# Kernel tuning notes

Hardware: AMD Instinct MI355X
Metric: run time of the kernel (lower is better)

The kernel has to match this reference:

```python
import jax, jax.numpy as jnp
import numpy as np

B, S, D = 2, 2048, 1024
H = 16
DH = D // H


def setup_inputs() -> dict:
    key = jax.random.key(0)
    ks = jax.random.split(key, 6)
    scale = 0.02
    X = jax.random.normal(ks[0], (B, S, D), dtype=jnp.float32)
    W_q = jax.random.normal(ks[1], (D, D), dtype=jnp.float32) * scale
    W_k = jax.random.normal(ks[2], (D, D), dtype=jnp.float32) * scale
    W_v = jax.random.normal(ks[3], (D, D), dtype=jnp.float32) * scale
    W_o = jax.random.normal(ks[4], (D, D), dtype=jnp.float32) * scale
    b_o = jax.random.normal(ks[5], (D,), dtype=jnp.float32) * scale
    return {"X": X, "W_q": W_q, "W_k": W_k, "W_v": W_v, "W_o": W_o, "b_o": b_o}


def reference(X, W_q, W_k, W_v, W_o, b_o):
    batch, seq, _ = X.shape
    # project and split heads -> [B, H, S, DH]
    Q = (X @ W_q).reshape(batch, seq, H, DH).transpose(0, 2, 1, 3)
    K = (X @ W_k).reshape(batch, seq, H, DH).transpose(0, 2, 1, 3)
    V = (X @ W_v).reshape(batch, seq, H, DH).transpose(0, 2, 1, 3)
    # scores [B, H, S, S]
    scores = jnp.einsum("bhqd,bhkd->bhqk", Q, K)
    causal = jnp.tril(jnp.ones((seq, seq), dtype=bool))  # True = keep
    scores = jnp.where(causal, scores, -jnp.inf)
    scores = scores / jnp.sqrt(jnp.float32(DH))
    weights = jax.nn.softmax(scores, axis=-1)
    # dropout_p = 0.0 -> identity
    ctx = jnp.einsum("bhqk,bhkd->bhqd", weights, V)
    ctx = ctx.transpose(0, 2, 1, 3).reshape(batch, seq, D)
    return ctx @ W_o + b_o
```

## Files before the change

### kernel.cpp

```cpp
#include <hip/hip_runtime.h>
#include <hip/hip_bf16.h>

#define S 2048
#define D 1024
#define NH 16
#define DH 64
#define M_TOT 4096

typedef float f32x4 __attribute__((ext_vector_type(4)));
typedef float f32x16 __attribute__((ext_vector_type(16)));
typedef __bf16 bf16x8 __attribute__((ext_vector_type(8)));

static __device__ __forceinline__ ushort f2bf(float f) {
    unsigned u = __float_as_uint(f);
    u += 0x7fffu + ((u >> 16) & 1u);
    return (ushort)(u >> 16);
}

static __device__ __forceinline__ int cvtpk_bf16(float lo, float hi) {
    int r;
    asm("v_cvt_pk_bf16_f32 %0, %1, %2" : "=v"(r) : "v"(lo), "v"(hi));
    return r;
}

static __device__ __forceinline__ void plswap(int& a, int& b) {
    asm("v_permlane32_swap_b32 %0, %1" : "+v"(a), "+v"(b));
}

static __device__ __forceinline__ float xhalf_add(float x) {
    return x + __shfl_xor(x, 32);
}

static __device__ __forceinline__ void gload16(const ushort* g, ushort* l) {
    __builtin_amdgcn_global_load_lds(
        (const __attribute__((address_space(1))) void*)g,
        (__attribute__((address_space(3))) void*)l, 16, 0, 0);
}

template<int N> static __device__ __forceinline__ void waitvm() {
    if constexpr (N == 0) asm volatile("s_waitcnt vmcnt(0)" ::: "memory");
    else if constexpr (N == 3) asm volatile("s_waitcnt vmcnt(3)" ::: "memory");
    else if constexpr (N == 4) asm volatile("s_waitcnt vmcnt(4)" ::: "memory");
}
static __device__ __forceinline__ void waitlgkm0() {
    asm volatile("s_waitcnt lgkmcnt(0)" ::: "memory");
}
static __device__ __forceinline__ void rawbar() {
    __builtin_amdgcn_s_barrier();
    __builtin_amdgcn_sched_barrier(0);
}

__global__ void k_convert(const float* __restrict__ src, ushort* __restrict__ dst, int n4) {
    int i = blockIdx.x * blockDim.x + threadIdx.x;
    int stride = gridDim.x * blockDim.x;
    for (int idx = i; idx < n4; idx += stride) {
        float4 v = ((const float4*)src)[idx];
        ushort4 o;
        o.x = f2bf(v.x); o.y = f2bf(v.y); o.z = f2bf(v.z); o.w = f2bf(v.w);
        ((ushort4*)dst)[idx] = o;
    }
}

__global__ void k_transposeW(const float* __restrict__ w0, const float* __restrict__ w1,
                             const float* __restrict__ w2, ushort* __restrict__ dst,
                             float scale0) {
    __shared__ float tile[32][33];
    int z = blockIdx.z;
    const float* src = (z == 0) ? w0 : (z == 1) ? w1 : w2;
    float scl = (z == 0) ? scale0 : 1.0f;
    int zoff = z * 1024;
    int bn = blockIdx.x * 32;
    int bk = blockIdx.y * 32;
    int tx = threadIdx.x & 31, ty = threadIdx.x >> 5;
    #pragma unroll
    for (int i = 0; i < 32; i += 8)
        tile[ty + i][tx] = src[(size_t)(bk + ty + i) * D + bn + tx];
    __syncthreads();
    #pragma unroll
    for (int i = 0; i < 32; i += 8)
        dst[(size_t)(zoff + bn + ty + i) * D + bk + tx] = f2bf(tile[tx][ty + i] * scl);
}

template<int MF>
__global__ __launch_bounds__(256) void k_gemm(
    const ushort* __restrict__ A, const ushort* __restrict__ Bt,
    ushort* __restrict__ Qd, ushort* __restrict__ Kd, ushort* __restrict__ Vd,
    float* __restrict__ Od, const float* __restrict__ bias, int mode)
{
    constexpr int BM = MF * 32;
    constexpr int ASZ = BM * 32;
    constexpr int BSZ = 128 * 32;
    constexpr int NL = (MF == 4) ? 4 : 3;
    __shared__ ushort SH[2 * ASZ + 2 * BSZ];
    ushort* As = SH;
    ushort* Bs = SH + 2 * ASZ;

    int tid = threadIdx.x, wave = tid >> 6, lane = tid & 63;
    int wm = (wave >> 1) * (MF * 16), wn = (wave & 1) * 64;
    int bm = blockIdx.x * BM, bn0 = blockIdx.y * 128;
    int lr = lane & 15, lk = (lane >> 4) * 8;
    int rr = (lane >> 4) * 4;
    f32x4 acc[MF][4] = {};

    const ushort* Ap0 = A + (size_t)(bm + (tid >> 2)) * D + (tid & 3) * 8;
    const ushort* Ap1 = A + (size_t)(bm + ((tid + 256) >> 2)) * D + (tid & 3) * 8;
    const ushort* Bp0 = Bt + (size_t)(bn0 + (tid >> 2)) * D + (tid & 3) * 8;
    const ushort* Bp1 = Bt + (size_t)(bn0 + ((tid + 256) >> 2)) * D + (tid & 3) * 8;
    ushort* la0 = As + tid * 8;
    ushort* la1 = As + (tid + 256) * 8;
    ushort* lb0 = Bs + tid * 8;
    ushort* lb1 = Bs + (tid + 256) * 8;

    auto stage = [&](int k, int buf) {
        int go = k * 32;
        gload16(Ap0 + go, la0 + buf * ASZ);
        if constexpr (MF == 4) gload16(Ap1 + go, la1 + buf * ASZ);
        gload16(Bp0 + go, lb0 + buf * BSZ);
        gload16(Bp1 + go, lb1 + buf * BSZ);
    };

    constexpr int NK = D / 32;
    stage(0, 0);
    stage(1, 1);

    #pragma unroll 1
    for (int k0 = 0; k0 < NK; ++k0) {
        if (k0 + 1 < NK) waitvm<NL>(); else waitvm<0>();
        rawbar();
        const ushort* Ac = As + (k0 & 1) * ASZ;
        const ushort* Bc = Bs + (k0 & 1) * BSZ;
        bf16x8 af[MF], bfr[4];
        #pragma unroll
        for (int m = 0; m < MF; ++m) af[m] = *(const bf16x8*)&Ac[(wm + m * 16 + lr) * 32 + lk];
        #pragma unroll
        for (int n = 0; n < 4; ++n) bfr[n] = *(const bf16x8*)&Bc[(wn + n * 16 + lr) * 32 + lk];
        waitlgkm0();
        rawbar();
        if (k0 + 2 < NK) stage(k0 + 2, k0 & 1);
        __builtin_amdgcn_s_setprio(1);
        #pragma unroll
        for (int m = 0; m < MF; ++m)
            #pragma unroll
            for (int n = 0; n < 4; ++n)
                acc[m][n] = __builtin_amdgcn_mfma_f32_16x16x32_bf16(af[m], bfr[n], acc[m][n], 0, 0, 0);
        __builtin_amdgcn_s_setprio(0);
    }

    if (mode == 0) {
        ushort* E = SH;
        const bool isV = (blockIdx.y >= 16);
        ushort* DstQK = (blockIdx.y < 8) ? Qd : Kd;
        int bnc = (blockIdx.y & 7) * 128;
        int b = bm >> 11;
        #pragma unroll 1
        for (int hh2 = 0; hh2 < 2; ++hh2) {
            __syncthreads();
            if (wm == hh2 * 64) {
                if (!isV) {
                    #pragma unroll
                    for (int m = 0; m < MF; ++m)
                        #pragma unroll
                        for (int n = 0; n < 4; ++n)
                            #pragma unroll
                            for (int r = 0; r < 4; ++r)
                                E[(m * 16 + rr + r) * 136 + wn + n * 16 + lr] = f2bf(acc[m][n][r]);
                } else {
                    #pragma unroll
                    for (int m = 0; m < MF; ++m)
                        #pragma unroll
                        for (int n = 0; n < 4; ++n) {
                            ushort4 w;
                            w.x = f2bf(acc[m][n][0]); w.y = f2bf(acc[m][n][1]);
                            w.z = f2bf(acc[m][n][2]); w.w = f2bf(acc[m][n][3]);
                            *(ushort4*)&E[(wn + n * 16 + lr) * 72 + m * 16 + rr] = w;
                        }
                }
            }
            __syncthreads();
            if (!isV) {
                #pragma unroll
                for (int p = 0; p < 4; ++p) {
                    int rloc = (tid >> 4) + p * 16;
                    int c8 = (tid & 15) * 8;
                    int4 v = *(const int4*)&E[rloc * 136 + c8];
                    int gm = bm + hh2 * 64 + rloc;
                    int ss = gm & (S - 1);
                    int n = bnc + c8;
                    int hh = n >> 6, dd = n & 63;
                    *(int4*)&DstQK[((size_t)(b * NH + hh) * S + ss) * DH + dd] = v;
                }
            } else {
                #pragma unroll
                for (int p = 0; p < 4; ++p) {
                    int c = tid >> 1;
                    int chunk = 2 * p + (tid & 1);
                    int4 v = *(const int4*)&E[c * 72 + chunk * 8];
                    int n = bnc + c;
                    int hh = n >> 6, dd = n & 63;
                    int gm = bm + hh2 * 64 + chunk * 8;
                    int ss = gm & (S - 1);
                    *(int4*)&Vd[((size_t)(b * NH + hh) * DH + dd) * S + ss] = v;
                }
            }
        }
    } else {
        #pragma unroll
        for (int m = 0; m < MF; ++m) {
            #pragma unroll
            for (int n = 0; n < 4; ++n) {
                int gn = bn0 + wn + n * 16 + lr;
                float bv = bias[gn];
                #pragma unroll
                for (int r = 0; r < 4; ++r) {
                    int gm = bm + wm + m * 16 + rr + r;
                    Od[(size_t)gm * D + gn] = acc[m][n][r] + bv;
                }
            }
        }
    }
}

__global__ __launch_bounds__(256, 4) void k_attn(
    const ushort* __restrict__ Qh, const ushort* __restrict__ Kh,
    const ushort* __restrict__ Vt, ushort* __restrict__ ctx)
{
    __shared__ ushort Ks[2][4096];
    __shared__ ushort Vs[2][4096];

    int bid = blockIdx.x;
    int r_ = bid >> 8, c_ = bid & 255;
    int qt = (r_ & 1) ? (c_ >> 3) : 31 - (c_ >> 3);
    int bh = (c_ & 7) + 8 * r_;

    int tid = threadIdx.x;
    int wave = tid >> 6, lane = tid & 63;
    int lo5 = lane & 31, hi = lane >> 5;
    int qs = wave >> 1, kp = wave & 1;
    int rxl = lo5 & 7;
    int b = bh >> 4, h = bh & (NH - 1);

    const ushort* Qp = Qh + (size_t)bh * S * DH;
    const ushort* Kp = Kh + (size_t)bh * S * DH;
    const ushort* Vp = Vt + (size_t)bh * DH * S;

    int q0 = qt * 64, q0w = q0 + qs * 32, qg = q0w + lo5;
    int nt = qt + 1;

    bf16x8 qf[4];
    #pragma unroll
    for (int ks = 0; ks < 4; ++ks)
        qf[ks] = *(const bf16x8*)&Qp[(size_t)qg * DH + ks * 16 + hi * 8];

    int koff[4], vof[2];
    #pragma unroll
    for (int ks = 0; ks < 4; ++ks)
        koff[ks] = (kp * 32 + lo5) * 64 + (((2 * ks + hi) ^ rxl) << 3);
    #pragma unroll
    for (int kc = 0; kc < 2; ++kc)
        vof[kc] = lo5 * 64 + (((kp * 4 + 2 * kc + hi) ^ rxl) << 3);

    int p0 = tid, p1 = tid + 256;
    int kr0 = p0 >> 3, kc0 = ((p0 & 7) ^ (kr0 & 7)) << 3;
    int kr1 = p1 >> 3, kc1 = ((p1 & 7) ^ (kr1 & 7)) << 3;
    const ushort* gkA = Kp + (size_t)kr0 * DH + kc0;
    const ushort* gkB = Kp + (size_t)kr1 * DH + kc1;
    const ushort* gvA = Vp + (size_t)kr0 * S + kc0;
    const ushort* gvB = Vp + (size_t)kr1 * S + kc1;
    ushort* lk0 = &Ks[0][p0 * 8];
    ushort* lk1 = &Ks[0][p1 * 8];
    ushort* lv0 = &Vs[0][p0 * 8];
    ushort* lv1 = &Vs[0][p1 * 8];

    auto stage = [&](int t, int buf) {
        int ko = t * (64 * DH);
        int vo = t * 64;
        int lo = buf * 4096;
        gload16(gkA + ko, lk0 + lo);
        gload16(gkB + ko, lk1 + lo);
        gload16(gvA + vo, lv0 + lo);
        gload16(gvB + vo, lv1 + lo);
    };

    f32x16 oacc[2] = {};
    float l = 0.f;

    stage(0, 0);
    if (nt > 1) stage(1, 1);

    #pragma unroll 1
    for (int t = 0; t < nt; ++t) {
        if (t + 1 < nt) waitvm<4>(); else waitvm<0>();
        rawbar();
        bool fullmask = (t == qt) && (kp == 1) && (qs == 0);
        if (!fullmask) {
            const ushort* KsC = &Ks[t & 1][0];
            const ushort* VsC = &Vs[t & 1][0];
            f32x16 sc = (f32x16)(0.f);
            __builtin_amdgcn_s_setprio(1);
            #pragma unroll
            for (int ks = 0; ks < 4; ++ks) {
                bf16x8 kf = *(const bf16x8*)&KsC[koff[ks]];
                sc = __builtin_amdgcn_mfma_f32_32x32x16_bf16(kf, qf[ks], sc, 0, 0, 0);
            }
            __builtin_amdgcn_s_setprio(0);

            int kv0 = t * 64;
            if (t == qt && !(kp == 0 && qs == 1)) {
                #pragma unroll
                for (int r2 = 0; r2 < 16; ++r2) {
                    int kvg = kv0 + kp * 32 + ((r2 & 3) + 8 * (r2 >> 2) + 4 * hi);
                    sc[r2] = (kvg > qg) ? -1e30f : sc[r2];
                }
            }
            float sum = 0.f;
            #pragma unroll
            for (int r2 = 0; r2 < 16; ++r2) {
                float p = exp2f(sc[r2]);
                sc[r2] = p;
                sum += p;
            }
            l += sum;

            bf16x8 pb[2];
            {
                int a0 = cvtpk_bf16(sc[0], sc[1]);
                int b0 = cvtpk_bf16(sc[4], sc[5]);
                plswap(a0, b0);
                int a1 = cvtpk_bf16(sc[2], sc[3]);
                int b1 = cvtpk_bf16(sc[6], sc[7]);
                plswap(a1, b1);
                int4 w0; w0.x = a0; w0.y = a1; w0.z = b0; w0.w = b1;
                pb[0] = *(bf16x8*)&w0;
                int a2 = cvtpk_bf16(sc[8], sc[9]);
                int b2 = cvtpk_bf16(sc[12], sc[13]);
                plswap(a2, b2);
                int a3 = cvtpk_bf16(sc[10], sc[11]);
                int b3 = cvtpk_bf16(sc[14], sc[15]);
                plswap(a3, b3);
                int4 w1; w1.x = a2; w1.y = a3; w1.z = b2; w1.w = b3;
                pb[1] = *(bf16x8*)&w1;
            }

            __builtin_amdgcn_s_setprio(1);
            #pragma unroll
            for (int kc = 0; kc < 2; ++kc) {
                bf16x8 vf0 = *(const bf16x8*)&VsC[vof[kc]];
                oacc[0] = __builtin_amdgcn_mfma_f32_32x32x16_bf16(vf0, pb[kc], oacc[0], 0, 0, 0);
                bf16x8 vf1 = *(const bf16x8*)&VsC[vof[kc] + 32 * 64];
                oacc[1] = __builtin_amdgcn_mfma_f32_32x32x16_bf16(vf1, pb[kc], oacc[1], 0, 0, 0);
            }
            __builtin_amdgcn_s_setprio(0);
        }
        waitlgkm0();
        rawbar();
        if (t + 2 < nt) stage(t + 2, t & 1);
    }

    l = xhalf_add(l);

    float4* scr4 = (float4*)&Ks[0][0];
    float* ls = (float*)&Vs[0][0];
    int row = qs * 64 + lane;
    if (kp == 1) {
        #pragma unroll
        for (int sub = 0; sub < 2; ++sub)
            #pragma unroll
            for (int cc = 0; cc < 4; ++cc) {
                float4 v4;
                v4.x = oacc[sub][4 * cc + 0];
                v4.y = oacc[sub][4 * cc + 1];
                v4.z = oacc[sub][4 * cc + 2];
                v4.w = oacc[sub][4 * cc + 3];
                scr4[row * 8 + ((sub * 4 + cc) ^ (row & 7))] = v4;
            }
        ls[row] = l;
    }
    __syncthreads();
    if (kp == 0) {
        float inv = 1.0f / (l + ls[row]);
        ushort* cp = ctx + (size_t)(b * S + qg) * D + h * DH;
        #pragma unroll
        for (int sub = 0; sub < 2; ++sub) {
            #pragma unroll
            for (int cc = 0; cc < 4; ++cc) {
                float4 v4 = scr4[row * 8 + ((sub * 4 + cc) ^ (row & 7))];
                float o0 = (oacc[sub][4 * cc + 0] + v4.x) * inv;
                float o1 = (oacc[sub][4 * cc + 1] + v4.y) * inv;
                float o2 = (oacc[sub][4 * cc + 2] + v4.z) * inv;
                float o3 = (oacc[sub][4 * cc + 3] + v4.w) * inv;
                int dh = 8 * cc + 4 * hi + 32 * sub;
                int2 w2; w2.x = cvtpk_bf16(o0, o1); w2.y = cvtpk_bf16(o2, o3);
                *(int2*)&cp[dh] = w2;
            }
        }
    }
}

extern "C" void kernel_launch(void* const* d_in, const int* in_sizes, int n_in,
                              void* d_out, int out_size, void* d_ws, size_t ws_size,
                              hipStream_t stream) {
    const float* X   = (const float*)d_in[0];
    const float* W_q = (const float*)d_in[1];
    const float* W_k = (const float*)d_in[2];
    const float* W_v = (const float*)d_in[3];
    const float* W_o = (const float*)d_in[4];
    const float* b_o = (const float*)d_in[5];
    float* out = (float*)d_out;

    ushort* Xb    = (ushort*)d_ws;
    ushort* Wqkvt = Xb    + (size_t)M_TOT * D;
    ushort* Wot   = Wqkvt + (size_t)3 * D * D;
    ushort* Qh    = Wot   + (size_t)D * D;
    ushort* Kh    = Qh    + (size_t)M_TOT * D;
    ushort* Vtr   = Kh    + (size_t)M_TOT * D;
    ushort* Ctx   = Vtr   + (size_t)M_TOT * D;

    k_convert<<<dim3(2048), dim3(256), 0, stream>>>(X, Xb, M_TOT * D / 4);
    k_transposeW<<<dim3(32, 32, 3), dim3(256), 0, stream>>>(W_q, W_k, W_v, Wqkvt, 0.18033688011112042f);
    k_transposeW<<<dim3(32, 32, 1), dim3(256), 0, stream>>>(W_o, W_o, W_o, Wot, 1.0f);

    k_gemm<4><<<dim3(32, 24), dim3(256), 0, stream>>>(Xb, Wqkvt, Qh, Kh, Vtr, nullptr, nullptr, 0);

    k_attn<<<dim3(1024), dim3(256), 0, stream>>>(Qh, Kh, Vtr, Ctx);

    k_gemm<2><<<dim3(64, 8), dim3(256), 0, stream>>>(Ctx, Wot, nullptr, nullptr, nullptr, out, b_o, 1);
}
```

Measured before the change: 114.0 us.

## Load K and V fragments directly from global memory instead of LDS staging

The attention loop drops the double-buffered LDS staging of K and V tiles, and with it the per-iteration barriers. Each wave now reads its MFMA K and V fragments straight from global memory, relying on the cache for reuse across waves. The exp-sum reduction becomes a tree. This removes the barrier and LDS traffic but exposes global load latency every iteration with no prefetching, and duplicates K/V loads across waves.

```diff
diff --git a/kernel.cpp b/kernel.cpp
--- a/kernel.cpp
+++ b/kernel.cpp
@@ -224,8 +224,8 @@
     const ushort* __restrict__ Qh, const ushort* __restrict__ Kh,
     const ushort* __restrict__ Vt, ushort* __restrict__ ctx)
 {
-    __shared__ ushort Ks[2][4096];
-    __shared__ ushort Vs[2][4096];
+    __shared__ float4 scr4[128 * 8];
+    __shared__ float ls[128];
 
     int bid = blockIdx.x;
     int r_ = bid >> 8, c_ = bid & 255;
@@ -236,7 +236,6 @@
     int wave = tid >> 6, lane = tid & 63;
     int lo5 = lane & 31, hi = lane >> 5;
     int qs = wave >> 1, kp = wave & 1;
-    int rxl = lo5 & 7;
     int b = bh >> 4, h = bh & (NH - 1);
 
     const ushort* Qp = Qh + (size_t)bh * S * DH;
@@ -251,115 +250,82 @@
     for (int ks = 0; ks < 4; ++ks)
         qf[ks] = *(const bf16x8*)&Qp[(size_t)qg * DH + ks * 16 + hi * 8];
 
-    int koff[4], vof[2];
-    #pragma unroll
-    for (int ks = 0; ks < 4; ++ks)
-        koff[ks] = (kp * 32 + lo5) * 64 + (((2 * ks + hi) ^ rxl) << 3);
-    #pragma unroll
-    for (int kc = 0; kc < 2; ++kc)
-        vof[kc] = lo5 * 64 + (((kp * 4 + 2 * kc + hi) ^ rxl) << 3);
-
-    int p0 = tid, p1 = tid + 256;
-    int kr0 = p0 >> 3, kc0 = ((p0 & 7) ^ (kr0 & 7)) << 3;
-    int kr1 = p1 >> 3, kc1 = ((p1 & 7) ^ (kr1 & 7)) << 3;
-    const ushort* gkA = Kp + (size_t)kr0 * DH + kc0;
-    const ushort* gkB = Kp + (size_t)kr1 * DH + kc1;
-    const ushort* gvA = Vp + (size_t)kr0 * S + kc0;
-    const ushort* gvB = Vp + (size_t)kr1 * S + kc1;
-    ushort* lk0 = &Ks[0][p0 * 8];
-    ushort* lk1 = &Ks[0][p1 * 8];
-    ushort* lv0 = &Vs[0][p0 * 8];
-    ushort* lv1 = &Vs[0][p1 * 8];
-
-    auto stage = [&](int t, int buf) {
-        int ko = t * (64 * DH);
-        int vo = t * 64;
-        int lo = buf * 4096;
-        gload16(gkA + ko, lk0 + lo);
-        gload16(gkB + ko, lk1 + lo);
-        gload16(gvA + vo, lv0 + lo);
-        gload16(gvB + vo, lv1 + lo);
-    };
+    const ushort* kb  = Kp + (size_t)(kp * 32 + lo5) * DH + hi * 8;
+    const ushort* vb0 = Vp + (size_t)lo5 * S + kp * 32 + hi * 8;
+    const ushort* vb1 = Vp + (size_t)(32 + lo5) * S + kp * 32 + hi * 8;
 
     f32x16 oacc[2] = {};
     float l = 0.f;
 
-    stage(0, 0);
-    if (nt > 1) stage(1, 1);
-
     #pragma unroll 1
     for (int t = 0; t < nt; ++t) {
-        if (t + 1 < nt) waitvm<4>(); else waitvm<0>();
-        rawbar();
         bool fullmask = (t == qt) && (kp == 1) && (qs == 0);
-        if (!fullmask) {
-            const ushort* KsC = &Ks[t & 1][0];
-            const ushort* VsC = &Vs[t & 1][0];
-            f32x16 sc = (f32x16)(0.f);
-            __builtin_amdgcn_s_setprio(1);
-            #pragma unroll
-            for (int ks = 0; ks < 4; ++ks) {
-                bf16x8 kf = *(const bf16x8*)&KsC[koff[ks]];
-                sc = __builtin_amdgcn_mfma_f32_32x32x16_bf16(kf, qf[ks], sc, 0, 0, 0);
-            }
-            __builtin_amdgcn_s_setprio(0);
-
-            int kv0 = t * 64;
-            if (t == qt && !(kp == 0 && qs == 1)) {
-                #pragma unroll
-                for (int r2 = 0; r2 < 16; ++r2) {
-                    int kvg = kv0 + kp * 32 + ((r2 & 3) + 8 * (r2 >> 2) + 4 * hi);
-                    sc[r2] = (kvg > qg) ? -1e30f : sc[r2];
-                }
-            }
-            float sum = 0.f;
+        if (fullmask) continue;
+        int kv0 = t * 64;
+
+        const ushort* kt = kb + (size_t)kv0 * DH;
+        bf16x8 kf0 = *(const bf16x8*)(kt);
+        bf16x8 kf1 = *(const bf16x8*)(kt + 16);
+        bf16x8 kf2 = *(const bf16x8*)(kt + 32);
+        bf16x8 kf3 = *(const bf16x8*)(kt + 48);
+        bf16x8 vf00 = *(const bf16x8*)(vb0 + kv0);
+        bf16x8 vf01 = *(const bf16x8*)(vb0 + kv0 + 16);
+        bf16x8 vf10 = *(const bf16x8*)(vb1 + kv0);
+        bf16x8 vf11 = *(const bf16x8*)(vb1 + kv0 + 16);
+
+        f32x16 sc = (f32x16)(0.f);
+        __builtin_amdgcn_s_setprio(1);
+        sc = __builtin_amdgcn_mfma_f32_32x32x16_bf16(kf0, qf[0], sc, 0, 0, 0);
+        sc = __builtin_amdgcn_mfma_f32_32x32x16_bf16(kf1, qf[1], sc, 0, 0, 0);
+        sc = __builtin_amdgcn_mfma_f32_32x32x16_bf16(kf2, qf[2], sc, 0, 0, 0);
+        sc = __builtin_amdgcn_mfma_f32_32x32x16_bf16(kf3, qf[3], sc, 0, 0, 0);
+        __builtin_amdgcn_s_setprio(0);
+
+        if (t == qt && !(kp == 0 && qs == 1)) {
             #pragma unroll
             for (int r2 = 0; r2 < 16; ++r2) {
-                float p = exp2f(sc[r2]);
-                sc[r2] = p;
-                sum += p;
-            }
-            l += sum;
-
-            bf16x8 pb[2];
-            {
-                int a0 = cvtpk_bf16(sc[0], sc[1]);
-                int b0 = cvtpk_bf16(sc[4], sc[5]);
-                plswap(a0, b0);
-                int a1 = cvtpk_bf16(sc[2], sc[3]);
-                int b1 = cvtpk_bf16(sc[6], sc[7]);
-                plswap(a1, b1);
-                int4 w0; w0.x = a0; w0.y = a1; w0.z = b0; w0.w = b1;
-                pb[0] = *(bf16x8*)&w0;
-                int a2 = cvtpk_bf16(sc[8], sc[9]);
-                int b2 = cvtpk_bf16(sc[12], sc[13]);
-                plswap(a2, b2);
-                int a3 = cvtpk_bf16(sc[10], sc[11]);
-                int b3 = cvtpk_bf16(sc[14], sc[15]);
-                plswap(a3, b3);
-                int4 w1; w1.x = a2; w1.y = a3; w1.z = b2; w1.w = b3;
-                pb[1] = *(bf16x8*)&w1;
-            }
-
-            __builtin_amdgcn_s_setprio(1);
-            #pragma unroll
-            for (int kc = 0; kc < 2; ++kc) {
-                bf16x8 vf0 = *(const bf16x8*)&VsC[vof[kc]];
-                oacc[0] = __builtin_amdgcn_mfma_f32_32x32x16_bf16(vf0, pb[kc], oacc[0], 0, 0, 0);
-                bf16x8 vf1 = *(const bf16x8*)&VsC[vof[kc] + 32 * 64];
-                oacc[1] = __builtin_amdgcn_mfma_f32_32x32x16_bf16(vf1, pb[kc], oacc[1], 0, 0, 0);
-            }
-            __builtin_amdgcn_s_setprio(0);
-        }
-        waitlgkm0();
-        rawbar();
-        if (t + 2 < nt) stage(t + 2, t & 1);
+                int kvg = kv0 + kp * 32 + ((r2 & 3) + 8 * (r2 >> 2) + 4 * hi);
+                sc[r2] = (kvg > qg) ? -1e30f : sc[r2];
+            }
+        }
+        #pragma unroll
+        for (int r2 = 0; r2 < 16; ++r2)
+            sc[r2] = exp2f(sc[r2]);
+        float t0 = sc[0] + sc[1], t1 = sc[2] + sc[3], t2 = sc[4] + sc[5], t3 = sc[6] + sc[7];
+        float t4 = sc[8] + sc[9], t5 = sc[10] + sc[11], t6 = sc[12] + sc[13], t7 = sc[14] + sc[15];
+        float u0 = t0 + t1, u1 = t2 + t3, u2 = t4 + t5, u3 = t6 + t7;
+        l += (u0 + u1) + (u2 + u3);
+
+        bf16x8 pb[2];
+        {
+            int a0 = cvtpk_bf16(sc[0], sc[1]);
+            int b0 = cvtpk_bf16(sc[4], sc[5]);
+            plswap(a0, b0);
+            int a1 = cvtpk_bf16(sc[2], sc[3]);
+            int b1 = cvtpk_bf16(sc[6], sc[7]);
+            plswap(a1, b1);
+            int4 w0; w0.x = a0; w0.y = a1; w0.z = b0; w0.w = b1;
+            pb[0] = *(bf16x8*)&w0;
+            int a2 = cvtpk_bf16(sc[8], sc[9]);
+            int b2 = cvtpk_bf16(sc[12], sc[13]);
+            plswap(a2, b2);
+            int a3 = cvtpk_bf16(sc[10], sc[11]);
+            int b3 = cvtpk_bf16(sc[14], sc[15]);
+            plswap(a3, b3);
+            int4 w1; w1.x = a2; w1.y = a3; w1.z = b2; w1.w = b3;
+            pb[1] = *(bf16x8*)&w1;
+        }
+
+        __builtin_amdgcn_s_setprio(1);
+        oacc[0] = __builtin_amdgcn_mfma_f32_32x32x16_bf16(vf00, pb[0], oacc[0], 0, 0, 0);
+        oacc[0] = __builtin_amdgcn_mfma_f32_32x32x16_bf16(vf01, pb[1], oacc[0], 0, 0, 0);
+        oacc[1] = __builtin_amdgcn_mfma_f32_32x32x16_bf16(vf10, pb[0], oacc[1], 0, 0, 0);
+        oacc[1] = __builtin_amdgcn_mfma_f32_32x32x16_bf16(vf11, pb[1], oacc[1], 0, 0, 0);
+        __builtin_amdgcn_s_setprio(0);
     }
 
     l = xhalf_add(l);
 
-    float4* scr4 = (float4*)&Ks[0][0];
-    float* ls = (float*)&Vs[0][0];
     int row = qs * 64 + lane;
     if (kp == 1) {
         #pragma unroll
```

New measurement: 135.9 us. 19.2% more time.

## Restructure causal attention into 512-thread blocks processing paired query tiles

Applied to the files above, without the earlier changes.

The attention kernel now launches 256 blocks of 512 threads. Each block handles 128-row query tiles, and each block processes two tiles, one from the front and one from the back of the causal triangle, so every block gets an equal amount of work. Each block has 8 waves, and every thread stages one K and one V chunk per tile instead of two. Work is skipped per wave with a general causal test. The change is meant to balance causal load across a single wave of blocks and to cut per-block launch overhead, at the cost of fewer resident blocks and more per-thread sequential work.

```diff
diff --git a/kernel.cpp b/kernel.cpp
--- a/kernel.cpp
+++ b/kernel.cpp
@@ -39,6 +39,7 @@
 
 template<int N> static __device__ __forceinline__ void waitvm() {
     if constexpr (N == 0) asm volatile("s_waitcnt vmcnt(0)" ::: "memory");
+    else if constexpr (N == 2) asm volatile("s_waitcnt vmcnt(2)" ::: "memory");
     else if constexpr (N == 3) asm volatile("s_waitcnt vmcnt(3)" ::: "memory");
     else if constexpr (N == 4) asm volatile("s_waitcnt vmcnt(4)" ::: "memory");
 }
@@ -220,36 +221,28 @@
     }
 }
 
-__global__ __launch_bounds__(256, 4) void k_attn(
+__global__ __launch_bounds__(512) void k_attn(
     const ushort* __restrict__ Qh, const ushort* __restrict__ Kh,
     const ushort* __restrict__ Vt, ushort* __restrict__ ctx)
 {
-    __shared__ ushort Ks[2][4096];
-    __shared__ ushort Vs[2][4096];
+    __shared__ ushort SH[2 * 4096 * 2 + 512];
+    ushort* Ks = SH;
+    ushort* Vs = SH + 8192;
 
     int bid = blockIdx.x;
-    int r_ = bid >> 8, c_ = bid & 255;
-    int qt = (r_ & 1) ? (c_ >> 3) : 31 - (c_ >> 3);
-    int bh = (c_ & 7) + 8 * r_;
+    int y = bid >> 5;
+    int bh = ((bid & 7) << 2) | ((bid >> 3) & 3);
+    int b = bh >> 4, h = bh & (NH - 1);
 
     int tid = threadIdx.x;
     int wave = tid >> 6, lane = tid & 63;
     int lo5 = lane & 31, hi = lane >> 5;
     int qs = wave >> 1, kp = wave & 1;
     int rxl = lo5 & 7;
-    int b = bh >> 4, h = bh & (NH - 1);
 
     const ushort* Qp = Qh + (size_t)bh * S * DH;
     const ushort* Kp = Kh + (size_t)bh * S * DH;
     const ushort* Vp = Vt + (size_t)bh * DH * S;
-
-    int q0 = qt * 64, q0w = q0 + qs * 32, qg = q0w + lo5;
-    int nt = qt + 1;
-
-    bf16x8 qf[4];
-    #pragma unroll
-    for (int ks = 0; ks < 4; ++ks)
-        qf[ks] = *(const bf16x8*)&Qp[(size_t)qg * DH + ks * 16 + hi * 8];
 
     int koff[4], vof[2];
     #pragma unroll
@@ -259,140 +252,141 @@
     for (int kc = 0; kc < 2; ++kc)
         vof[kc] = lo5 * 64 + (((kp * 4 + 2 * kc + hi) ^ rxl) << 3);
 
-    int p0 = tid, p1 = tid + 256;
-    int kr0 = p0 >> 3, kc0 = ((p0 & 7) ^ (kr0 & 7)) << 3;
-    int kr1 = p1 >> 3, kc1 = ((p1 & 7) ^ (kr1 & 7)) << 3;
+    int kr0 = tid >> 3, kc0 = ((tid & 7) ^ (kr0 & 7)) << 3;
     const ushort* gkA = Kp + (size_t)kr0 * DH + kc0;
-    const ushort* gkB = Kp + (size_t)kr1 * DH + kc1;
     const ushort* gvA = Vp + (size_t)kr0 * S + kc0;
-    const ushort* gvB = Vp + (size_t)kr1 * S + kc1;
-    ushort* lk0 = &Ks[0][p0 * 8];
-    ushort* lk1 = &Ks[0][p1 * 8];
-    ushort* lv0 = &Vs[0][p0 * 8];
-    ushort* lv1 = &Vs[0][p1 * 8];
+    ushort* lk0 = &Ks[tid * 8];
+    ushort* lv0 = &Vs[tid * 8];
 
     auto stage = [&](int t, int buf) {
-        int ko = t * (64 * DH);
-        int vo = t * 64;
-        int lo = buf * 4096;
-        gload16(gkA + ko, lk0 + lo);
-        gload16(gkB + ko, lk1 + lo);
-        gload16(gvA + vo, lv0 + lo);
-        gload16(gvB + vo, lv1 + lo);
+        gload16(gkA + (size_t)t * (64 * DH), lk0 + buf * 4096);
+        gload16(gvA + t * 64, lv0 + buf * 4096);
     };
 
-    f32x16 oacc[2] = {};
-    float l = 0.f;
-
-    stage(0, 0);
-    if (nt > 1) stage(1, 1);
-
     #pragma unroll 1
-    for (int t = 0; t < nt; ++t) {
-        if (t + 1 < nt) waitvm<4>(); else waitvm<0>();
-        rawbar();
-        bool fullmask = (t == qt) && (kp == 1) && (qs == 0);
-        if (!fullmask) {
-            const ushort* KsC = &Ks[t & 1][0];
-            const ushort* VsC = &Vs[t & 1][0];
-            f32x16 sc = (f32x16)(0.f);
-            __builtin_amdgcn_s_setprio(1);
+    for (int half = 0; half < 2; ++half) {
+        int u = half ? y : (15 - y);
+        int q0w = u * 128 + qs * 32;
+        int qg = q0w + lo5;
+        int nt = 2 * u + 2;
+
+        bf16x8 qf[4];
+        #pragma unroll
+        for (int ks = 0; ks < 4; ++ks)
+            qf[ks] = *(const bf16x8*)&Qp[(size_t)qg * DH + ks * 16 + hi * 8];
+
+        f32x16 oacc[2] = {};
+        float l = 0.f;
+
+        stage(0, 0);
+        if (nt > 1) stage(1, 1);
+
+        #pragma unroll 1
+        for (int t = 0; t < nt; ++t) {
+            if (t + 1 < nt) waitvm<2>(); else waitvm<0>();
+            rawbar();
+            int kvbase = t * 64 + kp * 32;
+            bool skip = kvbase > q0w + 31;
+            if (!skip) {
+                const ushort* KsC = &Ks[(t & 1) * 4096];
+                const ushort* VsC = &Vs[(t & 1) * 4096];
+                f32x16 sc = (f32x16)(0.f);
+                __builtin_amdgcn_s_setprio(1);
+                #pragma unroll
+                for (int ks = 0; ks < 4; ++ks) {
+                    bf16x8 kf = *(const bf16x8*)&KsC[koff[ks]];
+                    sc = __builtin_amdgcn_mfma_f32_32x32x16_bf16(kf, qf[ks], sc, 0, 0, 0);
+                }
+                __builtin_amdgcn_s_setprio(0);
+
+                if (kvbase + 31 > q0w) {
+                    #pragma unroll
+                    for (int r2 = 0; r2 < 16; ++r2) {
+                        int kvg = kvbase + ((r2 & 3) + 8 * (r2 >> 2) + 4 * hi);
+                        sc[r2] = (kvg > qg) ? -1e30f : sc[r2];
+                    }
+                }
+                #pragma unroll
+                for (int r2 = 0; r2 < 16; ++r2)
+                    sc[r2] = exp2f(sc[r2]);
+                float t0 = sc[0] + sc[1], t1 = sc[2] + sc[3], t2 = sc[4] + sc[5], t3 = sc[6] + sc[7];
+                float t4 = sc[8] + sc[9], t5 = sc[10] + sc[11], t6 = sc[12] + sc[13], t7 = sc[14] + sc[15];
+                l += ((t0 + t1) + (t2 + t3)) + ((t4 + t5) + (t6 + t7));
+
+                bf16x8 pb[2];
+                {
+                    int a0 = cvtpk_bf16(sc[0], sc[1]);
+                    int b0 = cvtpk_bf16(sc[4], sc[5]);
+                    plswap(a0, b0);
+                    int a1 = cvtpk_bf16(sc[2], sc[3]);
+                    int b1 = cvtpk_bf16(sc[6], sc[7]);
+                    plswap(a1, b1);
+                    int4 w0; w0.x = a0; w0.y = a1; w0.z = b0; w0.w = b1;
+                    pb[0] = *(bf16x8*)&w0;
+                    int a2 = cvtpk_bf16(sc[8], sc[9]);
+                    int b2 = cvtpk_bf16(sc[12], sc[13]);
+                    plswap(a2, b2);
+                    int a3 = cvtpk_bf16(sc[10], sc[11]);
+                    int b3 = cvtpk_bf16(sc[14], sc[15]);
+                    plswap(a3, b3);
+                    int4 w1; w1.x = a2; w1.y = a3; w1.z = b2; w1.w = b3;
+                    pb[1] = *(bf16x8*)&w1;
+                }
+
+                __builtin_amdgcn_s_setprio(1);
+                #pragma unroll
+                for (int kc = 0; kc < 2; ++kc) {
+                    bf16x8 vf0 = *(const bf16x8*)&VsC[vof[kc]];
+                    oacc[0] = __builtin_amdgcn_mfma_f32_32x32x16_bf16(vf0, pb[kc], oacc[0], 0, 0, 0);
+                    bf16x8 vf1 = *(const bf16x8*)&VsC[vof[kc] + 32 * 64];
+                    oacc[1] = __builtin_amdgcn_mfma_f32_32x32x16_bf16(vf1, pb[kc], oacc[1], 0, 0, 0);
+                }
+                __builtin_amdgcn_s_setprio(0);
+            }
+            waitlgkm0();
+            rawbar();
+            if (t + 2 < nt) stage(t + 2, t & 1);
+        }
+
+        l = xhalf_add(l);
+
+        float4* scr4 = (float4*)SH;
+        float* ls = (float*)&SH[16384];
+        int row = qs * 64 + lane;
+        if (kp == 1) {
             #pragma unroll
-            for (int ks = 0; ks < 4; ++ks) {
-                bf16x8 kf = *(const bf16x8*)&KsC[koff[ks]];
-                sc = __builtin_amdgcn_mfma_f32_32x32x16_bf16(kf, qf[ks], sc, 0, 0, 0);
-            }
-            __builtin_amdgcn_s_setprio(0);
-
-            int kv0 = t * 64;
-            if (t == qt && !(kp == 0 && qs == 1)) {
-                #pragma unroll
-                for (int r2 = 0; r2 < 16; ++r2) {
-                    int kvg = kv0 + kp * 32 + ((r2 & 3) + 8 * (r2 >> 2) + 4 * hi);
-                    sc[r2] = (kvg > qg) ? -1e30f : sc[r2];
-                }
-            }
-            float sum = 0.f;
+            for (int sub = 0; sub < 2; ++sub)
+                #pragma unroll
+                for (int cc = 0; cc < 4; ++cc) {
+                    float4 v4;
+                    v4.x = oacc[sub][4 * cc + 0];
+                    v4.y = oacc[sub][4 * cc + 1];
+                    v4.z = oacc[sub][4 * cc + 2];
+                    v4.w = oacc[sub][4 * cc + 3];
+                    scr4[row * 8 + ((sub * 4 + cc) ^ (row & 7))] = v4;
+                }
+            ls[row] = l;
+        }
+        __syncthreads();
+        if (kp == 0) {
+            float inv = 1.0f / (l + ls[row]);
+            ushort* cp = ctx + (size_t)(b * S + qg) * D + h * DH;
             #pragma unroll
-            for (int r2 = 0; r2 < 16; ++r2) {
-                float p = exp2f(sc[r2]);
-                sc[r2] = p;
-                sum += p;
-            }
-            l += sum;
-
-            bf16x8 pb[2];
-            {
-                int a0 = cvtpk_bf16(sc[0], sc[1]);
-                int b0 = cvtpk_bf16(sc[4], sc[5]);
-                plswap(a0, b0);
-                int a1 = cvtpk_bf16(sc[2], sc[3]);
-                int b1 = cvtpk_bf16(sc[6], sc[7]);
-                plswap(a1, b1);
-                int4 w0; w0.x = a0; w0.y = a1; w0.z = b0; w0.w = b1;
-                pb[0] = *(bf16x8*)&w0;
-                int a2 = cvtpk_bf16(sc[8], sc[9]);
-                int b2 = cvtpk_bf16(sc[12], sc[13]);
-                plswap(a2, b2);
-                int a3 = cvtpk_bf16(sc[10], sc[11]);
-                int b3 = cvtpk_bf16(sc[14], sc[15]);
-                plswap(a3, b3);
-                int4 w1; w1.x = a2; w1.y = a3; w1.z = b2; w1.w = b3;
-                pb[1] = *(bf16x8*)&w1;
-            }
-
-            __builtin_amdgcn_s_setprio(1);
-            #pragma unroll
-            for (int kc = 0; kc < 2; ++kc) {
-                bf16x8 vf0 = *(const bf16x8*)&VsC[vof[kc]];
-                oacc[0] = __builtin_amdgcn_mfma_f32_32x32x16_bf16(vf0, pb[kc], oacc[0], 0, 0, 0);
-                bf16x8 vf1 = *(const bf16x8*)&VsC[vof[kc] + 32 * 64];
-                oacc[1] = __builtin_amdgcn_mfma_f32_32x32x16_bf16(vf1, pb[kc], oacc[1], 0, 0, 0);
-            }
-            __builtin_amdgcn_s_setprio(0);
-        }
-        waitlgkm0();
-        rawbar();
-        if (t + 2 < nt) stage(t + 2, t & 1);
-    }
-
-    l = xhalf_add(l);
-
-    float4* scr4 = (float4*)&Ks[0][0];
-    float* ls = (float*)&Vs[0][0];
-    int row = qs * 64 + lane;
-    if (kp == 1) {
-        #pragma unroll
-        for (int sub = 0; sub < 2; ++sub)
-            #pragma unroll
-            for (int cc = 0; cc < 4; ++cc) {
-                float4 v4;
-                v4.x = oacc[sub][4 * cc + 0];
-                v4.y = oacc[sub][4 * cc + 1];
-                v4.z = oacc[sub][4 * cc + 2];
-                v4.w = oacc[sub][4 * cc + 3];
-                scr4[row * 8 + ((sub * 4 + cc) ^ (row & 7))] = v4;
-            }
-        ls[row] = l;
-    }
-    __syncthreads();
-    if (kp == 0) {
-        float inv = 1.0f / (l + ls[row]);
-        ushort* cp = ctx + (size_t)(b * S + qg) * D + h * DH;
-        #pragma unroll
-        for (int sub = 0; sub < 2; ++sub) {
-            #pragma unroll
-            for (int cc = 0; cc < 4; ++cc) {
-                float4 v4 = scr4[row * 8 + ((sub * 4 + cc) ^ (row & 7))];
-                float o0 = (oacc[sub][4 * cc + 0] + v4.x) * inv;
-                float o1 = (oacc[sub][4 * cc + 1] + v4.y) * inv;
-                float o2 = (oacc[sub][4 * cc + 2] + v4.z) * inv;
-                float o3 = (oacc[sub][4 * cc + 3] + v4.w) * inv;
-                int dh = 8 * cc + 4 * hi + 32 * sub;
-                int2 w2; w2.x = cvtpk_bf16(o0, o1); w2.y = cvtpk_bf16(o2, o3);
-                *(int2*)&cp[dh] = w2;
+            for (int sub = 0; sub < 2; ++sub) {
+                #pragma unroll
+                for (int cc = 0; cc < 4; ++cc) {
+                    float4 v4 = scr4[row * 8 + ((sub * 4 + cc) ^ (row & 7))];
+                    float o0 = (oacc[sub][4 * cc + 0] + v4.x) * inv;
+                    float o1 = (oacc[sub][4 * cc + 1] + v4.y) * inv;
+                    float o2 = (oacc[sub][4 * cc + 2] + v4.z) * inv;
+                    float o3 = (oacc[sub][4 * cc + 3] + v4.w) * inv;
+                    int dh = 8 * cc + 4 * hi + 32 * sub;
+                    int2 w2; w2.x = cvtpk_bf16(o0, o1); w2.y = cvtpk_bf16(o2, o3);
+                    *(int2*)&cp[dh] = w2;
+                }
             }
         }
+        __syncthreads();
     }
 }
 
@@ -421,7 +415,7 @@
 
     k_gemm<4><<<dim3(32, 24), dim3(256), 0, stream>>>(Xb, Wqkvt, Qh, Kh, Vtr, nullptr, nullptr, 0);
 
-    k_attn<<<dim3(1024), dim3(256), 0, stream>>>(Qh, Kh, Vtr, Ctx);
+    k_attn<<<dim3(256), dim3(512), 0, stream>>>(Qh, Kh, Vtr, Ctx);
 
     k_gemm<2><<<dim3(64, 8), dim3(256), 0, stream>>>(Ctx, Wot, nullptr, nullptr, nullptr, out, b_o, 1);
 }
```

Result: slower. 116.6 us (+2.2%).

## Use triple-buffered LDS to drop second barrier in GEMM and attention loops

Applied to the files above, without the earlier changes.

Both the projection GEMM and the attention kernel move from double to triple LDS buffering. Each iteration can then issue the next prefetch right after the top barrier, and the trailing lgkmcnt wait plus second barrier go away. The attention kernel drops its occupancy hint from launch_bounds and sums the exponentials with a tree reduction instead of a serial chain. The extra LDS per block may lower occupancy, and a __syncthreads is added before the LDS scratch is reused in the epilogue.

```diff
diff --git a/kernel.cpp b/kernel.cpp
--- a/kernel.cpp
+++ b/kernel.cpp
@@ -41,9 +41,6 @@
     if constexpr (N == 0) asm volatile("s_waitcnt vmcnt(0)" ::: "memory");
     else if constexpr (N == 3) asm volatile("s_waitcnt vmcnt(3)" ::: "memory");
     else if constexpr (N == 4) asm volatile("s_waitcnt vmcnt(4)" ::: "memory");
-}
-static __device__ __forceinline__ void waitlgkm0() {
-    asm volatile("s_waitcnt lgkmcnt(0)" ::: "memory");
 }
 static __device__ __forceinline__ void rawbar() {
     __builtin_amdgcn_s_barrier();
@@ -91,9 +88,9 @@
     constexpr int ASZ = BM * 32;
     constexpr int BSZ = 128 * 32;
     constexpr int NL = (MF == 4) ? 4 : 3;
-    __shared__ ushort SH[2 * ASZ + 2 * BSZ];
+    __shared__ ushort SH[3 * ASZ + 3 * BSZ];
     ushort* As = SH;
-    ushort* Bs = SH + 2 * ASZ;
+    ushort* Bs = SH + 3 * ASZ;
 
     int tid = threadIdx.x, wave = tid >> 6, lane = tid & 63;
     int wm = (wave >> 1) * (MF * 16), wn = (wave & 1) * 64;
@@ -123,20 +120,20 @@
     stage(0, 0);
     stage(1, 1);
 
+    int cur = 0;
     #pragma unroll 1
     for (int k0 = 0; k0 < NK; ++k0) {
         if (k0 + 1 < NK) waitvm<NL>(); else waitvm<0>();
         rawbar();
-        const ushort* Ac = As + (k0 & 1) * ASZ;
-        const ushort* Bc = Bs + (k0 & 1) * BSZ;
+        int bs = cur + 2; if (bs >= 3) bs -= 3;
+        const ushort* Ac = As + cur * ASZ;
+        const ushort* Bc = Bs + cur * BSZ;
         bf16x8 af[MF], bfr[4];
         #pragma unroll
         for (int m = 0; m < MF; ++m) af[m] = *(const bf16x8*)&Ac[(wm + m * 16 + lr) * 32 + lk];
         #pragma unroll
         for (int n = 0; n < 4; ++n) bfr[n] = *(const bf16x8*)&Bc[(wn + n * 16 + lr) * 32 + lk];
-        waitlgkm0();
-        rawbar();
-        if (k0 + 2 < NK) stage(k0 + 2, k0 & 1);
+        if (k0 + 2 < NK) stage(k0 + 2, bs);
         __builtin_amdgcn_s_setprio(1);
         #pragma unroll
         for (int m = 0; m < MF; ++m)
@@ -144,6 +141,7 @@
             for (int n = 0; n < 4; ++n)
                 acc[m][n] = __builtin_amdgcn_mfma_f32_16x16x32_bf16(af[m], bfr[n], acc[m][n], 0, 0, 0);
         __builtin_amdgcn_s_setprio(0);
+        cur = (cur == 2) ? 0 : cur + 1;
     }
 
     if (mode == 0) {
@@ -220,12 +218,12 @@
     }
 }
 
-__global__ __launch_bounds__(256, 4) void k_attn(
+__global__ __launch_bounds__(256) void k_attn(
     const ushort* __restrict__ Qh, const ushort* __restrict__ Kh,
     const ushort* __restrict__ Vt, ushort* __restrict__ ctx)
 {
-    __shared__ ushort Ks[2][4096];
-    __shared__ ushort Vs[2][4096];
+    __shared__ ushort Ks[3 * 4096];
+    __shared__ ushort Vs[3 * 4096];
 
     int bid = blockIdx.x;
     int r_ = bid >> 8, c_ = bid & 255;
@@ -266,10 +264,10 @@
     const ushort* gkB = Kp + (size_t)kr1 * DH + kc1;
     const ushort* gvA = Vp + (size_t)kr0 * S + kc0;
     const ushort* gvB = Vp + (size_t)kr1 * S + kc1;
-    ushort* lk0 = &Ks[0][p0 * 8];
-    ushort* lk1 = &Ks[0][p1 * 8];
-    ushort* lv0 = &Vs[0][p0 * 8];
-    ushort* lv1 = &Vs[0][p1 * 8];
+    ushort* lk0 = &Ks[p0 * 8];
+    ushort* lk1 = &Ks[p1 * 8];
+    ushort* lv0 = &Vs[p0 * 8];
+    ushort* lv1 = &Vs[p1 * 8];
 
     auto stage = [&](int t, int buf) {
         int ko = t * (64 * DH);
@@ -287,14 +285,17 @@
     stage(0, 0);
     if (nt > 1) stage(1, 1);
 
+    int cur = 0;
     #pragma unroll 1
     for (int t = 0; t < nt; ++t) {
         if (t + 1 < nt) waitvm<4>(); else waitvm<0>();
         rawbar();
+        int bs = cur + 2; if (bs >= 3) bs -= 3;
+        if (t + 2 < nt) stage(t + 2, bs);
         bool fullmask = (t == qt) && (kp == 1) && (qs == 0);
         if (!fullmask) {
-            const ushort* KsC = &Ks[t & 1][0];
-            const ushort* VsC = &Vs[t & 1][0];
+            const ushort* KsC = &Ks[cur * 4096];
+            const ushort* VsC = &Vs[cur * 4096];
             f32x16 sc = (f32x16)(0.f);
             __builtin_amdgcn_s_setprio(1);
             #pragma unroll
@@ -312,14 +313,12 @@
                     sc[r2] = (kvg > qg) ? -1e30f : sc[r2];
                 }
             }
-            float sum = 0.f;
-            #pragma unroll
-            for (int r2 = 0; r2 < 16; ++r2) {
-                float p = exp2f(sc[r2]);
-                sc[r2] = p;
-                sum += p;
-            }
-            l += sum;
+            #pragma unroll
+            for (int r2 = 0; r2 < 16; ++r2)
+                sc[r2] = exp2f(sc[r2]);
+            float t0 = sc[0] + sc[1], t1 = sc[2] + sc[3], t2 = sc[4] + sc[5], t3 = sc[6] + sc[7];
+            float t4 = sc[8] + sc[9], t5 = sc[10] + sc[11], t6 = sc[12] + sc[13], t7 = sc[14] + sc[15];
+            l += ((t0 + t1) + (t2 + t3)) + ((t4 + t5) + (t6 + t7));
 
             bf16x8 pb[2];
             {
@@ -351,15 +350,15 @@
             }
             __builtin_amdgcn_s_setprio(0);
         }
-        waitlgkm0();
-        rawbar();
-        if (t + 2 < nt) stage(t + 2, t & 1);
+        cur = (cur == 2) ? 0 : cur + 1;
     }
 
     l = xhalf_add(l);
 
-    float4* scr4 = (float4*)&Ks[0][0];
-    float* ls = (float*)&Vs[0][0];
+    __syncthreads();
+
+    float4* scr4 = (float4*)&Ks[0];
+    float* ls = (float*)&Vs[0];
     int row = qs * 64 + lane;
     if (kp == 1) {
         #pragma unroll
```

New measurement: 135.2 us. 18.5% more time.
